# Kernel optimization log

Hardware: AMD Instinct MI355X
Metric: run time of the kernel (lower is better)

Reference implementation:

```python
import jax, jax.numpy as jnp
import numpy as np

N = 262144
D = 6
M = 6
EPS = 1e-05
ALPHA = 0.05


def _w(k, out_dim, in_dim):
    # Kaiming-uniform-ish init like torch Linear default
    bound = 1.0 / np.sqrt(in_dim)
    return jax.random.uniform(k, (out_dim, in_dim), jnp.float32, -bound, bound)


def _b(k, out_dim, in_dim):
    bound = 1.0 / np.sqrt(in_dim)
    return jax.random.uniform(k, (out_dim,), jnp.float32, -bound, bound)


def setup_inputs() -> dict:
    key = jax.random.key(0)
    ks = jax.random.split(key, 32)
    inp = {
        "X": jax.random.normal(ks[0], (N, D), jnp.float32),
        "U": jax.random.normal(ks[1], (N, M), jnp.float32),
        "xref": jax.random.normal(ks[2], (1, D), jnp.float32),
        # FNN: 6 -> 80 -> 200 -> 6
        "fnn_w1": _w(ks[3], 80, D), "fnn_b1": _b(ks[4], 80, D),
        "fnn_w2": _w(ks[5], 200, 80), "fnn_b2": _b(ks[6], 200, 80),
        "fnn_w3": _w(ks[7], D, 200), "fnn_b3": _b(ks[8], D, 200),
        # GNN: 6 -> 36
        "gnn_w": _w(ks[9], D * M, D), "gnn_b": _b(ks[10], D * M, D),
        # ICNN: 6 -> 60 -> 60 -> 30 -> 1 with input skips
        "icnn_w1": _w(ks[11], 60, D), "icnn_b1": _b(ks[12], 60, D),
        "icnn_w2": _w(ks[13], 60, 60), "icnn_b2": _b(ks[14], 60, 60),
        "icnn_w3": _w(ks[15], 30, 60), "icnn_b3": _b(ks[16], 30, 60),
        "icnn_w4": _w(ks[17], 1, 30), "icnn_b4": _b(ks[18], 1, 30),
        "icnn_im2": _w(ks[19], 60, D),
        "icnn_im3": _w(ks[20], 30, D),
        "icnn_im4": _w(ks[21], 1, D),
    }
    return inp


def reference(X, U, xref,
              fnn_w1, fnn_b1, fnn_w2, fnn_b2, fnn_w3, fnn_b3,
              gnn_w, gnn_b,
              icnn_w1, icnn_b1, icnn_w2, icnn_b2, icnn_w3, icnn_b3,
              icnn_w4, icnn_b4, icnn_im2, icnn_im3, icnn_im4):
    def lin(x, W, b=None):
        y = x @ W.T
        return y if b is None else y + b

    def icnn(x):  # (n, D) -> (n, 1)
        h = jax.nn.softplus(lin(x, icnn_w1, icnn_b1))
        h = jax.nn.softplus(lin(h, icnn_w2, icnn_b2) + lin(x, icnn_im2))
        h = jax.nn.softplus(lin(h, icnn_w3, icnn_b3) + lin(x, icnn_im3))
        return lin(h, icnn_w4, icnn_b4) + lin(x, icnn_im4)

    def V_fn(Xb):  # (n, D) -> (n,)
        h = icnn(Xb)[:, 0] - icnn(xref)[0, 0]
        # sigma(h) = (h>=1)(h-0.5) + (0<h<1)(0.5 h^2)
        sigma = jnp.where(h >= 1.0, h - 0.5,
                          jnp.where(h > 0.0, 0.5 * h * h, 0.0))
        dx = Xb - xref
        return sigma + EPS * jnp.sum(dx * dx, axis=1)

    # FNN (tanh hiddens)
    h = jnp.tanh(lin(X, fnn_w1, fnn_b1))
    h = jnp.tanh(lin(h, fnn_w2, fnn_b2))
    f_X = lin(h, fnn_w3, fnn_b3)  # (N, D)

    # GNN
    g_X = lin(X, gnn_w, gnn_b).reshape(X.shape[0], D, M)  # (N, D, M)

    # Lyapunov value and its gradient (per-sample, via grad of summed V)
    V = V_fn(X)  # (N,)
    dV = jax.grad(lambda Z: jnp.sum(V_fn(Z)))(X)  # (N, D)

    # Stability correction
    sc = jnp.sum(dV * f_X, axis=1) + ALPHA * V
    sc = sc - jnp.sum(jnp.abs(jnp.einsum('nd,ndm->nm', dV, g_X)), axis=1)
    dV_norm = dV / jnp.sum(dV * dV, axis=1, keepdims=True)
    f_cor = -dV_norm * jax.nn.relu(sc)[:, None]

    dX_opt = f_X + f_cor + jnp.einsum('ndm,nm->nd', g_X, U)
    return dX_opt
```

## Files before the change

### kernel.cpp

```cpp
#include <hip/hip_runtime.h>

#define EPS 1e-05f
#define ALPHA 0.05f

typedef _Float16 h2v __attribute__((ext_vector_type(2)));
typedef _Float16 f16x8 __attribute__((ext_vector_type(8)));
typedef float f32x16 __attribute__((ext_vector_type(16)));

__device__ __forceinline__ float rcp_f(float x){ return __builtin_amdgcn_rcpf(x); }
__device__ __forceinline__ float dot2(h2v a, h2v b, float c){
  return __builtin_amdgcn_fdot2(a, b, c, false);
}

#define LOG2E 1.4426950408889634f
#define LN2   0.6931471805599453f

__device__ __forceinline__ float fast_tanh(float x){
  float ax = fabsf(x);
  float e  = exp2f(ax * (-2.0f * LOG2E));
  float t  = (1.0f - e) * rcp_f(1.0f + e);
  return copysignf(t, x);
}
__device__ __forceinline__ float fast_sp(float x){
  float ax = fabsf(x);
  float e  = exp2f(ax * -LOG2E);
  return fmaxf(x, 0.0f) + log2f(1.0f + e) * LN2;
}
__device__ __forceinline__ float fast_sig(float x){
  float ax = fabsf(x);
  float e  = exp2f(ax * -LOG2E);
  float r  = rcp_f(1.0f + e);
  return x >= 0.0f ? r : e * r;
}
__device__ __forceinline__ float sig_from_sp(float sp){
  return 1.0f - exp2f(sp * -LOG2E);
}
__device__ __forceinline__ h2v mkh2(float a, float b){
  h2v r; r.x = (_Float16)a; r.y = (_Float16)b; return r;
}
__device__ __forceinline__ uint packh(float a, float b){
  ushort lo = __builtin_bit_cast(ushort, (_Float16)a);
  ushort hi = __builtin_bit_cast(ushort, (_Float16)b);
  return (uint)lo | ((uint)hi << 16);
}
__device__ __forceinline__ float f16lo(uint u){
  return (float)__builtin_bit_cast(_Float16, (ushort)(u & 0xffffu));
}
__device__ __forceinline__ float f16hi(uint u){
  return (float)__builtin_bit_cast(_Float16, (ushort)(u >> 16));
}

__global__ __launch_bounds__(512, 2) void holo_main(
    const float* __restrict__ X, const float* __restrict__ U,
    const float* __restrict__ xref,
    const float* __restrict__ fw1, const float* __restrict__ fb1,
    const float* __restrict__ fw2, const float* __restrict__ fb2,
    const float* __restrict__ fw3, const float* __restrict__ fb3,
    const float* __restrict__ gw,  const float* __restrict__ gb,
    const float* __restrict__ iw1, const float* __restrict__ ib1,
    const float* __restrict__ iw2, const float* __restrict__ ib2,
    const float* __restrict__ iw3, const float* __restrict__ ib3,
    const float* __restrict__ iw4, const float* __restrict__ ib4,
    const float* __restrict__ im2, const float* __restrict__ im3,
    const float* __restrict__ im4,
    float* __restrict__ out, int N)
{
  __shared__ ushort sW2r[224*84];
  __shared__ uint4  sW3r[224];
  __shared__ h2v sPW1[240];
  __shared__ h2v sPG[108];
  __shared__ h2v sPI1[180];
  __shared__ h2v sPI1C[180];
  __shared__ h2v sPI3[900];
  __shared__ h2v sPI3C[900];
  __shared__ h2v sPM2[180];
  __shared__ h2v sPM2C[180];
  __shared__ h2v sPM3[90];
  __shared__ h2v sPM3C[90];
  __shared__ h2v sPM4[4];
  __shared__ h2v sPI2T[1800];
  __shared__ h2v sPI2C[1800];
  __shared__ float sFB1[80], sFB3[6], sGB[36];
  __shared__ float sIB1[60], sIB2[60], sIB3[30], sIW4[30], sIM4[6], sXREF[6];
  __shared__ float sS1[60], sS2[60], sS3[30];
  __shared__ float sYREF, sIB4;

  const int t = threadIdx.x;
  const int T = 512;
  const int lane = t & 63;

  for (int idx=t; idx<224*42; idx+=T){
    int row = idx/42, c = idx%42, k = 2*c;
    uint v = 0;
    if (row < 200 && k < 80) v = packh(fw2[row*80+k], fw2[row*80+k+1]);
    ((uint*)sW2r)[idx] = v;
  }
  for (int n=t; n<224; n+=T){
    uint4 v = {0u,0u,0u,0u};
    if (n < 200){
      v.x = packh(fw3[0*200+n], fw3[1*200+n]);
      v.y = packh(fw3[2*200+n], fw3[3*200+n]);
      v.z = packh(fw3[4*200+n], fw3[5*200+n]);
      v.w = __builtin_bit_cast(uint, fb2[n]);
    }
    sW3r[n] = v;
  }
  for (int i=t;i<240;i+=T){ int o=i/3,p=i%3; sPW1[i]=mkh2(fw1[o*6+2*p],fw1[o*6+2*p+1]); }
  for (int i=t;i<108;i+=T){ int o=i/3,p=i%3; sPG[i]=mkh2(gw[o*6+2*p],gw[o*6+2*p+1]); }
  for (int i=t;i<180;i+=T){ int o=i/3,p=i%3; sPI1[i]=mkh2(iw1[o*6+2*p],iw1[o*6+2*p+1]); }
  for (int i=t;i<180;i+=T){ int q=i/6,d=i%6; sPI1C[i]=mkh2(iw1[(2*q)*6+d],iw1[(2*q+1)*6+d]); }
  for (int i=t;i<900;i+=T){ int r=i/30,q=i%30; sPI3[i]=mkh2(iw3[r*60+2*q],iw3[r*60+2*q+1]); }
  for (int i=t;i<900;i+=T){ int j=i/15,q=i%15; sPI3C[i]=mkh2(iw3[(2*q)*60+j],iw3[(2*q+1)*60+j]); }
  for (int i=t;i<180;i+=T){ int j=i/3,p=i%3; sPM2[i]=mkh2(im2[j*6+2*p],im2[j*6+2*p+1]); }
  for (int i=t;i<180;i+=T){ int q=i/6,d=i%6; sPM2C[i]=mkh2(im2[(2*q)*6+d],im2[(2*q+1)*6+d]); }
  for (int i=t;i<90;i+=T){ int r=i/3,p=i%3; sPM3[i]=mkh2(im3[r*6+2*p],im3[r*6+2*p+1]); }
  for (int i=t;i<90;i+=T){ int q=i/6,d=i%6; sPM3C[i]=mkh2(im3[(2*q)*6+d],im3[(2*q+1)*6+d]); }
  for (int i=t;i<3;i+=T) sPM4[i]=mkh2(im4[2*i],im4[2*i+1]);
  for (int i=t;i<1800;i+=T){ int p=i/60,j=i%60; sPI2T[i]=mkh2(iw2[j*60+2*p],iw2[j*60+2*p+1]); }
  for (int i=t;i<1800;i+=T){ int k1=i/30,q=i%30; sPI2C[i]=mkh2(iw2[(2*q)*60+k1],iw2[(2*q+1)*60+k1]); }
  for (int k=t;k<80;k+=T) sFB1[k]=fb1[k];
  for (int k=t;k<6;k+=T){ sFB3[k]=fb3[k]; sIM4[k]=im4[k]; sXREF[k]=xref[k]; }
  for (int k=t;k<36;k+=T) sGB[k]=gb[k];
  for (int k=t;k<60;k+=T){ sIB1[k]=ib1[k]; sIB2[k]=ib2[k]; }
  for (int k=t;k<30;k+=T){ sIB3[k]=ib3[k]; sIW4[k]=iw4[k]; }
  if (t==0) sIB4=ib4[0];
  __syncthreads();

  {
    h2v xrp[3];
    #pragma unroll
    for (int p = 0; p < 3; p++) xrp[p] = mkh2(sXREF[2*p], sXREF[2*p+1]);
    if (t < 60){
      float z = sIB1[t];
      #pragma unroll
      for (int p = 0; p < 3; p++) z = dot2(sPI1[t*3+p], xrp[p], z);
      sS1[t] = fast_sp(z);
    }
    __syncthreads();
    if (t < 60){
      float z = sIB2[t];
      #pragma unroll
      for (int p = 0; p < 3; p++) z = dot2(sPM2[t*3+p], xrp[p], z);
      for (int p = 0; p < 30; p++)
        z = dot2(sPI2T[p*60+t], mkh2(sS1[2*p], sS1[2*p+1]), z);
      sS2[t] = fast_sp(z);
    }
    __syncthreads();
    if (t < 30){
      float z = sIB3[t];
      #pragma unroll
      for (int p = 0; p < 3; p++) z = dot2(sPM3[t*3+p], xrp[p], z);
      for (int q = 0; q < 30; q++)
        z = dot2(sPI3[t*30+q], mkh2(sS2[2*q], sS2[2*q+1]), z);
      sS3[t] = fast_sp(z);
    }
    __syncthreads();
    if (t == 0){
      float y = sIB4;
      #pragma unroll
      for (int p = 0; p < 3; p++) y = dot2(sPM4[p], xrp[p], y);
      for (int j = 0; j < 30; j++) y = fmaf(sIW4[j], sS3[j], y);
      sYREF = y;
    }
    __syncthreads();
  }

  const int i = blockIdx.x * blockDim.x + t;
  const bool valid = (i < N);

  float x[6]; h2v xp[3];
  #pragma unroll
  for (int k = 0; k < 6; k++) x[k] = valid ? X[(long)i*6 + k] : 0.0f;
  #pragma unroll
  for (int p = 0; p < 3; p++) xp[p] = mkh2(x[2*p], x[2*p+1]);

  uint h1u[40];
  #pragma unroll
  for (int o = 0; o < 80; o += 2){
    float z0 = sFB1[o], z1 = sFB1[o+1];
    #pragma unroll
    for (int p = 0; p < 3; p++){
      z0 = dot2(sPW1[o*3 + p],     xp[p], z0);
      z1 = dot2(sPW1[(o+1)*3 + p], xp[p], z1);
    }
    h1u[o/2] = packh(fast_tanh(z0), fast_tanh(z1));
  }

  const int hh = lane >> 5;
  const int l31 = lane & 31;

  uint bf0[5][4], bf1[5][4];
  {
    int a0 = 4 * l31;
    int a1 = 4 * (32 + l31);
    #pragma unroll
    for (int kt = 0; kt < 5; kt++){
      #pragma unroll
      for (int q = 0; q < 4; q++){
        int lo0 = __builtin_amdgcn_ds_bpermute(a0, (int)h1u[kt*8 + q]);
        int hi0 = __builtin_amdgcn_ds_bpermute(a0, (int)h1u[kt*8 + 4 + q]);
        bf0[kt][q] = hh ? (uint)hi0 : (uint)lo0;
        int lo1 = __builtin_amdgcn_ds_bpermute(a1, (int)h1u[kt*8 + q]);
        int hi1 = __builtin_amdgcn_ds_bpermute(a1, (int)h1u[kt*8 + 4 + q]);
        bf1[kt][q] = hh ? (uint)hi1 : (uint)lo1;
      }
    }
  }

  float fp0[6] = {0.f,0.f,0.f,0.f,0.f,0.f};
  float fp1[6] = {0.f,0.f,0.f,0.f,0.f,0.f};
  for (int mt = 0; mt < 7; mt++){
    const int row = mt*32 + l31;
    f16x8 af[5];
    #pragma unroll
    for (int kt = 0; kt < 5; kt++){
      const ushort* wp = &sW2r[row*84 + kt*16 + 8*hh];
      uint2 w0 = *(const uint2*)wp;
      uint2 w1 = *(const uint2*)(wp + 4);
      uint4 au; au.x = w0.x; au.y = w0.y; au.z = w1.x; au.w = w1.y;
      af[kt] = __builtin_bit_cast(f16x8, au);
    }
    f32x16 acc0 = {0,0,0,0,0,0,0,0,0,0,0,0,0,0,0,0};
    f32x16 acc1 = {0,0,0,0,0,0,0,0,0,0,0,0,0,0,0,0};
    #pragma unroll
    for (int kt = 0; kt < 5; kt++){
      uint4 b0u; b0u.x=bf0[kt][0]; b0u.y=bf0[kt][1]; b0u.z=bf0[kt][2]; b0u.w=bf0[kt][3];
      uint4 b1u; b1u.x=bf1[kt][0]; b1u.y=bf1[kt][1]; b1u.z=bf1[kt][2]; b1u.w=bf1[kt][3];
      acc0 = __builtin_amdgcn_mfma_f32_32x32x16_f16(af[kt], __builtin_bit_cast(f16x8, b0u), acc0, 0, 0, 0);
      acc1 = __builtin_amdgcn_mfma_f32_32x32x16_f16(af[kt], __builtin_bit_cast(f16x8, b1u), acc1, 0, 0, 0);
    }
    #pragma unroll
    for (int reg = 0; reg < 16; reg++){
      int n = mt*32 + (reg & 3) + 8*(reg >> 2) + 4*hh;
      uint4 w = sW3r[n];
      float bias = __builtin_bit_cast(float, w.w);
      float t0 = fast_tanh(acc0[reg] + bias);
      float t1 = fast_tanh(acc1[reg] + bias);
      float w0 = f16lo(w.x), w1 = f16hi(w.x);
      float w2 = f16lo(w.y), w3 = f16hi(w.y);
      float w4 = f16lo(w.z), w5 = f16hi(w.z);
      fp0[0] = fmaf(w0, t0, fp0[0]); fp1[0] = fmaf(w0, t1, fp1[0]);
      fp0[1] = fmaf(w1, t0, fp0[1]); fp1[1] = fmaf(w1, t1, fp1[1]);
      fp0[2] = fmaf(w2, t0, fp0[2]); fp1[2] = fmaf(w2, t1, fp1[2]);
      fp0[3] = fmaf(w3, t0, fp0[3]); fp1[3] = fmaf(w3, t1, fp1[3]);
      fp0[4] = fmaf(w4, t0, fp0[4]); fp1[4] = fmaf(w4, t1, fp1[4]);
      fp0[5] = fmaf(w5, t0, fp0[5]); fp1[5] = fmaf(w5, t1, fp1[5]);
    }
  }
  float f[6];
  #pragma unroll
  for (int d = 0; d < 6; d++){
    float s0 = fp0[d] + __shfl_xor(fp0[d], 32, 64);
    float s1 = fp1[d] + __shfl_xor(fp1[d], 32, 64);
    f[d] = sFB3[d] + (hh ? s1 : s0);
  }

  float c2[60];
  #pragma unroll
  for (int j = 0; j < 60; j++){
    float z = sIB2[j];
    #pragma unroll
    for (int p = 0; p < 3; p++) z = dot2(sPM2[j*3 + p], xp[p], z);
    c2[j] = z;
  }
  for (int p = 0; p < 30; p++){
    float za = sIB1[2*p], zb = sIB1[2*p+1];
    #pragma unroll
    for (int q = 0; q < 3; q++){
      za = dot2(sPI1[(2*p)*3 + q],   xp[q], za);
      zb = dot2(sPI1[(2*p+1)*3 + q], xp[q], zb);
    }
    h2v s = mkh2(fast_sp(za), fast_sp(zb));
    #pragma unroll
    for (int j = 0; j < 60; j++) c2[j] = dot2(sPI2T[p*60 + j], s, c2[j]);
  }
  h2v c2p[30];
  #pragma unroll
  for (int j = 0; j < 60; j += 2)
    c2p[j/2] = mkh2(fast_sp(c2[j]), fast_sp(c2[j+1]));

  float y = sIB4;
  #pragma unroll
  for (int p = 0; p < 3; p++) y = dot2(sPM4[p], xp[p], y);
  float ac[6];
  #pragma unroll
  for (int d = 0; d < 6; d++) ac[d] = sIM4[d];
  float g3[30];
  #pragma unroll
  for (int i3 = 0; i3 < 30; i3++){
    float z = sIB3[i3];
    #pragma unroll
    for (int p = 0; p < 3; p++) z = dot2(sPM3[i3*3 + p], xp[p], z);
    #pragma unroll
    for (int q = 0; q < 30; q++) z = dot2(sPI3[i3*30 + q], c2p[q], z);
    float sp3 = fast_sp(z);
    float w4  = sIW4[i3];
    y = fmaf(w4, sp3, y);
    g3[i3] = w4 * sig_from_sp(sp3);
  }
  h2v g3p[15];
  #pragma unroll
  for (int q = 0; q < 15; q++) g3p[q] = mkh2(g3[2*q], g3[2*q+1]);
  #pragma unroll
  for (int q = 0; q < 15; q++){
    #pragma unroll
    for (int d = 0; d < 6; d++) ac[d] = dot2(sPM3C[q*6 + d], g3p[q], ac[d]);
  }

  h2v g2p[30];
  #pragma unroll
  for (int j = 0; j < 60; j += 2){
    float ta = 0.0f, tb = 0.0f;
    #pragma unroll
    for (int q = 0; q < 15; q++){
      ta = dot2(sPI3C[j*15 + q],     g3p[q], ta);
      tb = dot2(sPI3C[(j+1)*15 + q], g3p[q], tb);
    }
    h2v sp = c2p[j/2];
    ta *= sig_from_sp((float)sp.x);
    tb *= sig_from_sp((float)sp.y);
    h2v tp = mkh2(ta, tb);
    g2p[j/2] = tp;
    #pragma unroll
    for (int d = 0; d < 6; d++) ac[d] = dot2(sPM2C[(j/2)*6 + d], tp, ac[d]);
  }

  for (int p = 0; p < 30; p++){
    float za = sIB1[2*p], zb = sIB1[2*p+1];
    #pragma unroll
    for (int q = 0; q < 3; q++){
      za = dot2(sPI1[(2*p)*3 + q],   xp[q], za);
      zb = dot2(sPI1[(2*p+1)*3 + q], xp[q], zb);
    }
    float ta = 0.0f, tb = 0.0f;
    #pragma unroll
    for (int q = 0; q < 30; q++){
      ta = dot2(sPI2C[(2*p)*30 + q],   g2p[q], ta);
      tb = dot2(sPI2C[(2*p+1)*30 + q], g2p[q], tb);
    }
    ta *= fast_sig(za); tb *= fast_sig(zb);
    h2v tp = mkh2(ta, tb);
    #pragma unroll
    for (int d = 0; d < 6; d++) ac[d] = dot2(sPI1C[p*6 + d], tp, ac[d]);
  }

  float hdiff = y - sYREF;
  float sigma = (hdiff >= 1.0f) ? (hdiff - 0.5f) : ((hdiff > 0.0f) ? 0.5f*hdiff*hdiff : 0.0f);
  float sigp  = (hdiff >= 1.0f) ? 1.0f          : ((hdiff > 0.0f) ? hdiff             : 0.0f);
  float dx2 = 0.0f;
  float dV[6];
  #pragma unroll
  for (int d = 0; d < 6; d++){
    float dx = x[d] - sXREF[d];
    dx2 = fmaf(dx, dx, dx2);
    dV[d] = fmaf(sigp, ac[d], 2.0f*EPS*dx);
  }
  float V = sigma + EPS*dx2;

  float sc = ALPHA * V;
  #pragma unroll
  for (int d = 0; d < 6; d++) sc = fmaf(dV[d], f[d], sc);

  float u[6];
  #pragma unroll
  for (int m = 0; m < 6; m++) u[m] = valid ? U[(long)i*6 + m] : 0.0f;
  float am[6] = {0.f,0.f,0.f,0.f,0.f,0.f};
  float gU[6];
  #pragma unroll
  for (int d = 0; d < 6; d++){
    float acc = 0.0f;
    #pragma unroll
    for (int m = 0; m < 6; m++){
      int o = d*6 + m;
      float g = sGB[o];
      #pragma unroll
      for (int p = 0; p < 3; p++) g = dot2(sPG[o*3 + p], xp[p], g);
      am[m] = fmaf(dV[d], g, am[m]);
      acc   = fmaf(g, u[m], acc);
    }
    gU[d] = acc;
  }
  #pragma unroll
  for (int m = 0; m < 6; m++) sc -= fabsf(am[m]);

  float n2 = 0.0f;
  #pragma unroll
  for (int d = 0; d < 6; d++) n2 = fmaf(dV[d], dV[d], n2);
  float r = fmaxf(sc, 0.0f) * rcp_f(n2);

  if (valid){
    #pragma unroll
    for (int d = 0; d < 6; d++)
      out[(long)i*6 + d] = f[d] - dV[d]*r + gU[d];
  }
}

extern "C" void kernel_launch(void* const* d_in, const int* in_sizes, int n_in,
                              void* d_out, int out_size, void* d_ws, size_t ws_size,
                              hipStream_t stream)
{
  const float* X    = (const float*)d_in[0];
  const float* U    = (const float*)d_in[1];
  const float* xref = (const float*)d_in[2];
  const float* fw1  = (const float*)d_in[3];
  const float* fb1  = (const float*)d_in[4];
  const float* fw2  = (const float*)d_in[5];
  const float* fb2  = (const float*)d_in[6];
  const float* fw3  = (const float*)d_in[7];
  const float* fb3  = (const float*)d_in[8];
  const float* gw   = (const float*)d_in[9];
  const float* gb   = (const float*)d_in[10];
  const float* iw1  = (const float*)d_in[11];
  const float* ib1  = (const float*)d_in[12];
  const float* iw2  = (const float*)d_in[13];
  const float* ib2  = (const float*)d_in[14];
  const float* iw3  = (const float*)d_in[15];
  const float* ib3  = (const float*)d_in[16];
  const float* iw4  = (const float*)d_in[17];
  const float* ib4  = (const float*)d_in[18];
  const float* im2  = (const float*)d_in[19];
  const float* im3  = (const float*)d_in[20];
  const float* im4  = (const float*)d_in[21];

  float* out = (float*)d_out;
  int N = in_sizes[0] / 6;

  int threads = 512;
  int blocks  = (N + threads - 1) / threads;
  holo_main<<<blocks, threads, 0, stream>>>(X, U, xref,
      fw1, fb1, fw2, fb2, fw3, fb3, gw, gb,
      iw1, ib1, iw2, ib2, iw3, ib3, iw4, ib4, im2, im3, im4,
      out, N);
}
```

Baseline: 182.8 us.

## Repack shared-memory weights into 16-byte padded records for vectorized LDS reads

Repacks all small weight tables in LDS as padded uint4 records that carry their biases, so each row or bias group comes in with one 128-bit LDS load instead of many scalar 32-bit loads. The FNN output projection now packs tanh pairs into half2 and accumulates with fdot2, replacing scalar f16-to-f32 conversions and FMAs. This cuts LDS instruction count in the per-thread ICNN forward/backward chain. The cost is some zero padding in LDS and a longer one-time packing prologue per block.

```diff
diff --git a/kernel.cpp b/kernel.cpp
--- a/kernel.cpp
+++ b/kernel.cpp
@@ -11,6 +11,8 @@
 __device__ __forceinline__ float dot2(h2v a, h2v b, float c){
   return __builtin_amdgcn_fdot2(a, b, c, false);
 }
+__device__ __forceinline__ h2v uh(uint u){ return __builtin_bit_cast(h2v, u); }
+__device__ __forceinline__ float uf(uint u){ return __builtin_bit_cast(float, u); }
 
 #define LOG2E 1.4426950408889634f
 #define LN2   0.6931471805599453f
@@ -42,12 +44,6 @@
   ushort lo = __builtin_bit_cast(ushort, (_Float16)a);
   ushort hi = __builtin_bit_cast(ushort, (_Float16)b);
   return (uint)lo | ((uint)hi << 16);
-}
-__device__ __forceinline__ float f16lo(uint u){
-  return (float)__builtin_bit_cast(_Float16, (ushort)(u & 0xffffu));
-}
-__device__ __forceinline__ float f16hi(uint u){
-  return (float)__builtin_bit_cast(_Float16, (ushort)(u >> 16));
 }
 
 __global__ __launch_bounds__(512, 2) void holo_main(
@@ -65,23 +61,22 @@
     const float* __restrict__ im4,
     float* __restrict__ out, int N)
 {
-  __shared__ ushort sW2r[224*84];
-  __shared__ uint4  sW3r[224];
-  __shared__ h2v sPW1[240];
-  __shared__ h2v sPG[108];
-  __shared__ h2v sPI1[180];
-  __shared__ h2v sPI1C[180];
-  __shared__ h2v sPI3[900];
-  __shared__ h2v sPI3C[900];
-  __shared__ h2v sPM2[180];
-  __shared__ h2v sPM2C[180];
-  __shared__ h2v sPM3[90];
-  __shared__ h2v sPM3C[90];
-  __shared__ h2v sPM4[4];
-  __shared__ h2v sPI2T[1800];
-  __shared__ h2v sPI2C[1800];
-  __shared__ float sFB1[80], sFB3[6], sGB[36];
-  __shared__ float sIB1[60], sIB2[60], sIB3[30], sIW4[30], sIM4[6], sXREF[6];
+  __shared__ alignas(16) ushort sW2r[224*84];
+  __shared__ uint4 sW3E[224];
+  __shared__ uint4 sPW1B[80];
+  __shared__ uint4 sPGB[36];
+  __shared__ uint4 sPI1B[60];
+  __shared__ uint4 sPI1C[60];
+  __shared__ uint4 sPI3[240];
+  __shared__ uint4 sPI3C[240];
+  __shared__ uint4 sPM2B[60];
+  __shared__ uint4 sPM2C[60];
+  __shared__ uint4 sPM3B[60];
+  __shared__ uint4 sPM3C[30];
+  __shared__ uint  sPM4u[4];
+  __shared__ alignas(16) uint sPI2Tu[1800];
+  __shared__ uint4 sPI2C[480];
+  __shared__ float sFB3[6], sXREF[6], sIM4[6];
   __shared__ float sS1[60], sS2[60], sS3[30];
   __shared__ float sYREF, sIB4;
 
@@ -95,34 +90,75 @@
     if (row < 200 && k < 80) v = packh(fw2[row*80+k], fw2[row*80+k+1]);
     ((uint*)sW2r)[idx] = v;
   }
-  for (int n=t; n<224; n+=T){
-    uint4 v = {0u,0u,0u,0u};
+  for (int idx=t; idx<896; idx+=T){
+    int P = idx/8, c = idx%8, n = 2*P;
+    uint v = 0;
     if (n < 200){
-      v.x = packh(fw3[0*200+n], fw3[1*200+n]);
-      v.y = packh(fw3[2*200+n], fw3[3*200+n]);
-      v.z = packh(fw3[4*200+n], fw3[5*200+n]);
-      v.w = __builtin_bit_cast(uint, fb2[n]);
-    }
-    sW3r[n] = v;
-  }
-  for (int i=t;i<240;i+=T){ int o=i/3,p=i%3; sPW1[i]=mkh2(fw1[o*6+2*p],fw1[o*6+2*p+1]); }
-  for (int i=t;i<108;i+=T){ int o=i/3,p=i%3; sPG[i]=mkh2(gw[o*6+2*p],gw[o*6+2*p+1]); }
-  for (int i=t;i<180;i+=T){ int o=i/3,p=i%3; sPI1[i]=mkh2(iw1[o*6+2*p],iw1[o*6+2*p+1]); }
-  for (int i=t;i<180;i+=T){ int q=i/6,d=i%6; sPI1C[i]=mkh2(iw1[(2*q)*6+d],iw1[(2*q+1)*6+d]); }
-  for (int i=t;i<900;i+=T){ int r=i/30,q=i%30; sPI3[i]=mkh2(iw3[r*60+2*q],iw3[r*60+2*q+1]); }
-  for (int i=t;i<900;i+=T){ int j=i/15,q=i%15; sPI3C[i]=mkh2(iw3[(2*q)*60+j],iw3[(2*q+1)*60+j]); }
-  for (int i=t;i<180;i+=T){ int j=i/3,p=i%3; sPM2[i]=mkh2(im2[j*6+2*p],im2[j*6+2*p+1]); }
-  for (int i=t;i<180;i+=T){ int q=i/6,d=i%6; sPM2C[i]=mkh2(im2[(2*q)*6+d],im2[(2*q+1)*6+d]); }
-  for (int i=t;i<90;i+=T){ int r=i/3,p=i%3; sPM3[i]=mkh2(im3[r*6+2*p],im3[r*6+2*p+1]); }
-  for (int i=t;i<90;i+=T){ int q=i/6,d=i%6; sPM3C[i]=mkh2(im3[(2*q)*6+d],im3[(2*q+1)*6+d]); }
-  for (int i=t;i<3;i+=T) sPM4[i]=mkh2(im4[2*i],im4[2*i+1]);
-  for (int i=t;i<1800;i+=T){ int p=i/60,j=i%60; sPI2T[i]=mkh2(iw2[j*60+2*p],iw2[j*60+2*p+1]); }
-  for (int i=t;i<1800;i+=T){ int k1=i/30,q=i%30; sPI2C[i]=mkh2(iw2[(2*q)*60+k1],iw2[(2*q+1)*60+k1]); }
-  for (int k=t;k<80;k+=T) sFB1[k]=fb1[k];
+      if (c < 6)       v = packh(fw3[c*200+n], fw3[c*200+n+1]);
+      else if (c == 6) v = __builtin_bit_cast(uint, fb2[n]);
+      else             v = __builtin_bit_cast(uint, fb2[n+1]);
+    }
+    ((uint*)sW3E)[idx] = v;
+  }
+  for (int idx=t; idx<320; idx+=T){
+    int o = idx/4, c = idx%4;
+    ((uint*)sPW1B)[idx] = (c<3) ? packh(fw1[o*6+2*c], fw1[o*6+2*c+1])
+                                : __builtin_bit_cast(uint, fb1[o]);
+  }
+  for (int idx=t; idx<144; idx+=T){
+    int o = idx/4, c = idx%4;
+    ((uint*)sPGB)[idx] = (c<3) ? packh(gw[o*6+2*c], gw[o*6+2*c+1])
+                               : __builtin_bit_cast(uint, gb[o]);
+  }
+  for (int idx=t; idx<240; idx+=T){
+    int p = idx/8, c = idx%8, sub = c/4, cc = c%4, nr = 2*p+sub;
+    ((uint*)sPI1B)[idx] = (cc<3) ? packh(iw1[nr*6+2*cc], iw1[nr*6+2*cc+1])
+                                 : __builtin_bit_cast(uint, ib1[nr]);
+  }
+  for (int idx=t; idx<240; idx+=T){
+    int q = idx/8, c = idx%8;
+    ((uint*)sPI1C)[idx] = (c<6) ? packh(iw1[(2*q)*6+c], iw1[(2*q+1)*6+c]) : 0u;
+  }
+  for (int idx=t; idx<960; idx+=T){
+    int r = idx/32, q = idx%32;
+    ((uint*)sPI3)[idx] = (q<30) ? packh(iw3[r*60+2*q], iw3[r*60+2*q+1]) : 0u;
+  }
+  for (int idx=t; idx<960; idx+=T){
+    int j = idx/16, q = idx%16;
+    ((uint*)sPI3C)[idx] = (q<15) ? packh(iw3[(2*q)*60+j], iw3[(2*q+1)*60+j]) : 0u;
+  }
+  for (int idx=t; idx<240; idx+=T){
+    int j = idx/4, c = idx%4;
+    ((uint*)sPM2B)[idx] = (c<3) ? packh(im2[j*6+2*c], im2[j*6+2*c+1])
+                                : __builtin_bit_cast(uint, ib2[j]);
+  }
+  for (int idx=t; idx<240; idx+=T){
+    int q = idx/8, c = idx%8;
+    ((uint*)sPM2C)[idx] = (c<6) ? packh(im2[(2*q)*6+c], im2[(2*q+1)*6+c]) : 0u;
+  }
+  for (int idx=t; idx<240; idx+=T){
+    int r = idx/8, c = idx%8;
+    uint v = 0;
+    if (c < 3)       v = packh(im3[r*6+2*c], im3[r*6+2*c+1]);
+    else if (c == 3) v = __builtin_bit_cast(uint, ib3[r]);
+    else if (c == 4) v = __builtin_bit_cast(uint, iw4[r]);
+    ((uint*)sPM3B)[idx] = v;
+  }
+  for (int idx=t; idx<120; idx+=T){
+    int q = idx/8, c = idx%8;
+    ((uint*)sPM3C)[idx] = (c<6) ? packh(im3[(2*q)*6+c], im3[(2*q+1)*6+c]) : 0u;
+  }
+  for (int idx=t; idx<4; idx+=T)
+    sPM4u[idx] = (idx<3) ? packh(im4[2*idx], im4[2*idx+1]) : 0u;
+  for (int idx=t; idx<1800; idx+=T){
+    int p = idx/60, j = idx%60;
+    sPI2Tu[idx] = packh(iw2[j*60+2*p], iw2[j*60+2*p+1]);
+  }
+  for (int idx=t; idx<1920; idx+=T){
+    int k1 = idx/32, q = idx%32;
+    ((uint*)sPI2C)[idx] = (q<30) ? packh(iw2[(2*q)*60+k1], iw2[(2*q+1)*60+k1]) : 0u;
+  }
   for (int k=t;k<6;k+=T){ sFB3[k]=fb3[k]; sIM4[k]=im4[k]; sXREF[k]=xref[k]; }
-  for (int k=t;k<36;k+=T) sGB[k]=gb[k];
-  for (int k=t;k<60;k+=T){ sIB1[k]=ib1[k]; sIB2[k]=ib2[k]; }
-  for (int k=t;k<30;k+=T){ sIB3[k]=ib3[k]; sIW4[k]=iw4[k]; }
   if (t==0) sIB4=ib4[0];
   __syncthreads();
 
@@ -131,35 +167,39 @@
     #pragma unroll
     for (int p = 0; p < 3; p++) xrp[p] = mkh2(sXREF[2*p], sXREF[2*p+1]);
     if (t < 60){
-      float z = sIB1[t];
+      const uint* w = (const uint*)sPI1B + (t/2)*8 + (t&1)*4;
+      float z = uf(w[3]);
       #pragma unroll
-      for (int p = 0; p < 3; p++) z = dot2(sPI1[t*3+p], xrp[p], z);
+      for (int c = 0; c < 3; c++) z = dot2(uh(w[c]), xrp[c], z);
       sS1[t] = fast_sp(z);
     }
     __syncthreads();
     if (t < 60){
-      float z = sIB2[t];
+      const uint* m = (const uint*)sPM2B + t*4;
+      float z = uf(m[3]);
       #pragma unroll
-      for (int p = 0; p < 3; p++) z = dot2(sPM2[t*3+p], xrp[p], z);
+      for (int c = 0; c < 3; c++) z = dot2(uh(m[c]), xrp[c], z);
       for (int p = 0; p < 30; p++)
-        z = dot2(sPI2T[p*60+t], mkh2(sS1[2*p], sS1[2*p+1]), z);
+        z = dot2(uh(sPI2Tu[p*60+t]), mkh2(sS1[2*p], sS1[2*p+1]), z);
       sS2[t] = fast_sp(z);
     }
     __syncthreads();
     if (t < 30){
-      float z = sIB3[t];
+      const uint* m = (const uint*)sPM3B + t*8;
+      float z = uf(m[3]);
       #pragma unroll
-      for (int p = 0; p < 3; p++) z = dot2(sPM3[t*3+p], xrp[p], z);
+      for (int c = 0; c < 3; c++) z = dot2(uh(m[c]), xrp[c], z);
+      const uint* prow = (const uint*)sPI3 + t*32;
       for (int q = 0; q < 30; q++)
-        z = dot2(sPI3[t*30+q], mkh2(sS2[2*q], sS2[2*q+1]), z);
+        z = dot2(uh(prow[q]), mkh2(sS2[2*q], sS2[2*q+1]), z);
       sS3[t] = fast_sp(z);
     }
     __syncthreads();
     if (t == 0){
       float y = sIB4;
       #pragma unroll
-      for (int p = 0; p < 3; p++) y = dot2(sPM4[p], xrp[p], y);
-      for (int j = 0; j < 30; j++) y = fmaf(sIW4[j], sS3[j], y);
+      for (int p = 0; p < 3; p++) y = dot2(uh(sPM4u[p]), xrp[p], y);
+      for (int j = 0; j < 30; j++) y = fmaf(uf(((const uint*)sPM3B)[j*8+4]), sS3[j], y);
       sYREF = y;
     }
     __syncthreads();
@@ -177,12 +217,10 @@
   uint h1u[40];
   #pragma unroll
   for (int o = 0; o < 80; o += 2){
-    float z0 = sFB1[o], z1 = sFB1[o+1];
-    #pragma unroll
-    for (int p = 0; p < 3; p++){
-      z0 = dot2(sPW1[o*3 + p],     xp[p], z0);
-      z1 = dot2(sPW1[(o+1)*3 + p], xp[p], z1);
-    }
+    uint4 wa = sPW1B[o], wb = sPW1B[o+1];
+    float z0 = uf(wa.w), z1 = uf(wb.w);
+    z0 = dot2(uh(wa.x), xp[0], z0); z0 = dot2(uh(wa.y), xp[1], z0); z0 = dot2(uh(wa.z), xp[2], z0);
+    z1 = dot2(uh(wb.x), xp[0], z1); z1 = dot2(uh(wb.y), xp[1], z1); z1 = dot2(uh(wb.z), xp[2], z1);
     h1u[o/2] = packh(fast_tanh(z0), fast_tanh(z1));
   }
 
@@ -230,21 +268,22 @@
       acc1 = __builtin_amdgcn_mfma_f32_32x32x16_f16(af[kt], __builtin_bit_cast(f16x8, b1u), acc1, 0, 0, 0);
     }
     #pragma unroll
-    for (int reg = 0; reg < 16; reg++){
-      int n = mt*32 + (reg & 3) + 8*(reg >> 2) + 4*hh;
-      uint4 w = sW3r[n];
-      float bias = __builtin_bit_cast(float, w.w);
-      float t0 = fast_tanh(acc0[reg] + bias);
-      float t1 = fast_tanh(acc1[reg] + bias);
-      float w0 = f16lo(w.x), w1 = f16hi(w.x);
-      float w2 = f16lo(w.y), w3 = f16hi(w.y);
-      float w4 = f16lo(w.z), w5 = f16hi(w.z);
-      fp0[0] = fmaf(w0, t0, fp0[0]); fp1[0] = fmaf(w0, t1, fp1[0]);
-      fp0[1] = fmaf(w1, t0, fp0[1]); fp1[1] = fmaf(w1, t1, fp1[1]);
-      fp0[2] = fmaf(w2, t0, fp0[2]); fp1[2] = fmaf(w2, t1, fp1[2]);
-      fp0[3] = fmaf(w3, t0, fp0[3]); fp1[3] = fmaf(w3, t1, fp1[3]);
-      fp0[4] = fmaf(w4, t0, fp0[4]); fp1[4] = fmaf(w4, t1, fp1[4]);
-      fp0[5] = fmaf(w5, t0, fp0[5]); fp1[5] = fmaf(w5, t1, fp1[5]);
+    for (int c = 0; c < 4; c++){
+      #pragma unroll
+      for (int b0h = 0; b0h < 2; b0h++){
+        const int r0 = 4*c + 2*b0h;
+        const int P  = mt*16 + 4*c + 2*hh + b0h;
+        uint4 wa = sW3E[P*2], wb = sW3E[P*2+1];
+        float bA = uf(wb.z), bB = uf(wb.w);
+        h2v tp0 = mkh2(fast_tanh(acc0[r0] + bA), fast_tanh(acc0[r0+1] + bB));
+        h2v tp1 = mkh2(fast_tanh(acc1[r0] + bA), fast_tanh(acc1[r0+1] + bB));
+        fp0[0] = dot2(uh(wa.x), tp0, fp0[0]); fp1[0] = dot2(uh(wa.x), tp1, fp1[0]);
+        fp0[1] = dot2(uh(wa.y), tp0, fp0[1]); fp1[1] = dot2(uh(wa.y), tp1, fp1[1]);
+        fp0[2] = dot2(uh(wa.z), tp0, fp0[2]); fp1[2] = dot2(uh(wa.z), tp1, fp1[2]);
+        fp0[3] = dot2(uh(wa.w), tp0, fp0[3]); fp1[3] = dot2(uh(wa.w), tp1, fp1[3]);
+        fp0[4] = dot2(uh(wb.x), tp0, fp0[4]); fp1[4] = dot2(uh(wb.x), tp1, fp1[4]);
+        fp0[5] = dot2(uh(wb.y), tp0, fp0[5]); fp1[5] = dot2(uh(wb.y), tp1, fp1[5]);
+      }
     }
   }
   float f[6];
@@ -258,90 +297,136 @@
   float c2[60];
   #pragma unroll
   for (int j = 0; j < 60; j++){
-    float z = sIB2[j];
-    #pragma unroll
-    for (int p = 0; p < 3; p++) z = dot2(sPM2[j*3 + p], xp[p], z);
+    uint4 m = sPM2B[j];
+    float z = uf(m.w);
+    z = dot2(uh(m.x), xp[0], z); z = dot2(uh(m.y), xp[1], z); z = dot2(uh(m.z), xp[2], z);
     c2[j] = z;
   }
   for (int p = 0; p < 30; p++){
-    float za = sIB1[2*p], zb = sIB1[2*p+1];
-    #pragma unroll
-    for (int q = 0; q < 3; q++){
-      za = dot2(sPI1[(2*p)*3 + q],   xp[q], za);
-      zb = dot2(sPI1[(2*p+1)*3 + q], xp[q], zb);
-    }
+    uint4 wA = sPI1B[2*p], wB = sPI1B[2*p+1];
+    float za = uf(wA.w), zb = uf(wB.w);
+    za = dot2(uh(wA.x), xp[0], za); za = dot2(uh(wA.y), xp[1], za); za = dot2(uh(wA.z), xp[2], za);
+    zb = dot2(uh(wB.x), xp[0], zb); zb = dot2(uh(wB.y), xp[1], zb); zb = dot2(uh(wB.z), xp[2], zb);
     h2v s = mkh2(fast_sp(za), fast_sp(zb));
-    #pragma unroll
-    for (int j = 0; j < 60; j++) c2[j] = dot2(sPI2T[p*60 + j], s, c2[j]);
-  }
-  h2v c2p[30];
+    const uint* rowp = sPI2Tu + p*60;
+    #pragma unroll
+    for (int jj = 0; jj < 15; jj++){
+      uint4 v = *(const uint4*)(rowp + jj*4);
+      c2[4*jj+0] = dot2(uh(v.x), s, c2[4*jj+0]);
+      c2[4*jj+1] = dot2(uh(v.y), s, c2[4*jj+1]);
+      c2[4*jj+2] = dot2(uh(v.z), s, c2[4*jj+2]);
+      c2[4*jj+3] = dot2(uh(v.w), s, c2[4*jj+3]);
+    }
+  }
+  h2v c2p[32];
   #pragma unroll
   for (int j = 0; j < 60; j += 2)
     c2p[j/2] = mkh2(fast_sp(c2[j]), fast_sp(c2[j+1]));
+  c2p[30] = mkh2(0.f, 0.f); c2p[31] = mkh2(0.f, 0.f);
 
   float y = sIB4;
   #pragma unroll
-  for (int p = 0; p < 3; p++) y = dot2(sPM4[p], xp[p], y);
+  for (int p = 0; p < 3; p++) y = dot2(uh(sPM4u[p]), xp[p], y);
   float ac[6];
   #pragma unroll
   for (int d = 0; d < 6; d++) ac[d] = sIM4[d];
   float g3[30];
   #pragma unroll
   for (int i3 = 0; i3 < 30; i3++){
-    float z = sIB3[i3];
-    #pragma unroll
-    for (int p = 0; p < 3; p++) z = dot2(sPM3[i3*3 + p], xp[p], z);
-    #pragma unroll
-    for (int q = 0; q < 30; q++) z = dot2(sPI3[i3*30 + q], c2p[q], z);
+    uint4 m0 = sPM3B[2*i3], m1 = sPM3B[2*i3+1];
+    float z = uf(m0.w);
+    z = dot2(uh(m0.x), xp[0], z); z = dot2(uh(m0.y), xp[1], z); z = dot2(uh(m0.z), xp[2], z);
+    const uint4* prow = sPI3 + i3*8;
+    #pragma unroll
+    for (int q4 = 0; q4 < 8; q4++){
+      uint4 v = prow[q4];
+      z = dot2(uh(v.x), c2p[4*q4+0], z);
+      z = dot2(uh(v.y), c2p[4*q4+1], z);
+      z = dot2(uh(v.z), c2p[4*q4+2], z);
+      z = dot2(uh(v.w), c2p[4*q4+3], z);
+    }
     float sp3 = fast_sp(z);
-    float w4  = sIW4[i3];
+    float w4  = uf(m1.x);
     y = fmaf(w4, sp3, y);
     g3[i3] = w4 * sig_from_sp(sp3);
   }
-  h2v g3p[15];
+  h2v g3p[16];
   #pragma unroll
   for (int q = 0; q < 15; q++) g3p[q] = mkh2(g3[2*q], g3[2*q+1]);
+  g3p[15] = mkh2(0.f, 0.f);
   #pragma unroll
   for (int q = 0; q < 15; q++){
-    #pragma unroll
-    for (int d = 0; d < 6; d++) ac[d] = dot2(sPM3C[q*6 + d], g3p[q], ac[d]);
-  }
-
-  h2v g2p[30];
-  #pragma unroll
-  for (int j = 0; j < 60; j += 2){
+    uint4 a = sPM3C[2*q], b = sPM3C[2*q+1];
+    ac[0] = dot2(uh(a.x), g3p[q], ac[0]);
+    ac[1] = dot2(uh(a.y), g3p[q], ac[1]);
+    ac[2] = dot2(uh(a.z), g3p[q], ac[2]);
+    ac[3] = dot2(uh(a.w), g3p[q], ac[3]);
+    ac[4] = dot2(uh(b.x), g3p[q], ac[4]);
+    ac[5] = dot2(uh(b.y), g3p[q], ac[5]);
+  }
+
+  h2v g2p[32];
+  #pragma unroll
+  for (int jp = 0; jp < 30; jp++){
+    const uint4* r0p = sPI3C + (2*jp)*4;
+    const uint4* r1p = sPI3C + (2*jp+1)*4;
     float ta = 0.0f, tb = 0.0f;
     #pragma unroll
-    for (int q = 0; q < 15; q++){
-      ta = dot2(sPI3C[j*15 + q],     g3p[q], ta);
-      tb = dot2(sPI3C[(j+1)*15 + q], g3p[q], tb);
-    }
-    h2v sp = c2p[j/2];
+    for (int q4 = 0; q4 < 4; q4++){
+      uint4 v0 = r0p[q4], v1 = r1p[q4];
+      ta = dot2(uh(v0.x), g3p[4*q4+0], ta);
+      ta = dot2(uh(v0.y), g3p[4*q4+1], ta);
+      ta = dot2(uh(v0.z), g3p[4*q4+2], ta);
+      ta = dot2(uh(v0.w), g3p[4*q4+3], ta);
+      tb = dot2(uh(v1.x), g3p[4*q4+0], tb);
+      tb = dot2(uh(v1.y), g3p[4*q4+1], tb);
+      tb = dot2(uh(v1.z), g3p[4*q4+2], tb);
+      tb = dot2(uh(v1.w), g3p[4*q4+3], tb);
+    }
+    h2v sp = c2p[jp];
     ta *= sig_from_sp((float)sp.x);
     tb *= sig_from_sp((float)sp.y);
     h2v tp = mkh2(ta, tb);
-    g2p[j/2] = tp;
-    #pragma unroll
-    for (int d = 0; d < 6; d++) ac[d] = dot2(sPM2C[(j/2)*6 + d], tp, ac[d]);
-  }
+    g2p[jp] = tp;
+    uint4 a = sPM2C[2*jp], b = sPM2C[2*jp+1];
+    ac[0] = dot2(uh(a.x), tp, ac[0]);
+    ac[1] = dot2(uh(a.y), tp, ac[1]);
+    ac[2] = dot2(uh(a.z), tp, ac[2]);
+    ac[3] = dot2(uh(a.w), tp, ac[3]);
+    ac[4] = dot2(uh(b.x), tp, ac[4]);
+    ac[5] = dot2(uh(b.y), tp, ac[5]);
+  }
+  g2p[30] = mkh2(0.f, 0.f); g2p[31] = mkh2(0.f, 0.f);
 
   for (int p = 0; p < 30; p++){
-    float za = sIB1[2*p], zb = sIB1[2*p+1];
-    #pragma unroll
-    for (int q = 0; q < 3; q++){
-      za = dot2(sPI1[(2*p)*3 + q],   xp[q], za);
-      zb = dot2(sPI1[(2*p+1)*3 + q], xp[q], zb);
-    }
+    uint4 wA = sPI1B[2*p], wB = sPI1B[2*p+1];
+    float za = uf(wA.w), zb = uf(wB.w);
+    za = dot2(uh(wA.x), xp[0], za); za = dot2(uh(wA.y), xp[1], za); za = dot2(uh(wA.z), xp[2], za);
+    zb = dot2(uh(wB.x), xp[0], zb); zb = dot2(uh(wB.y), xp[1], zb); zb = dot2(uh(wB.z), xp[2], zb);
+    const uint4* c0 = sPI2C + (2*p)*8;
+    const uint4* c1 = sPI2C + (2*p+1)*8;
     float ta = 0.0f, tb = 0.0f;
     #pragma unroll
-    for (int q = 0; q < 30; q++){
-      ta = dot2(sPI2C[(2*p)*30 + q],   g2p[q], ta);
-      tb = dot2(sPI2C[(2*p+1)*30 + q], g2p[q], tb);
+    for (int q4 = 0; q4 < 8; q4++){
+      uint4 v0 = c0[q4], v1 = c1[q4];
+      ta = dot2(uh(v0.x), g2p[4*q4+0], ta);
+      ta = dot2(uh(v0.y), g2p[4*q4+1], ta);
+      ta = dot2(uh(v0.z), g2p[4*q4+2], ta);
+      ta = dot2(uh(v0.w), g2p[4*q4+3], ta);
+      tb = dot2(uh(v1.x), g2p[4*q4+0], tb);
+      tb = dot2(uh(v1.y), g2p[4*q4+1], tb);
+      tb = dot2(uh(v1.z), g2p[4*q4+2], tb);
+      tb = dot2(uh(v1.w), g2p[4*q4+3], tb);
     }
     ta *= fast_sig(za); tb *= fast_sig(zb);
     h2v tp = mkh2(ta, tb);
-    #pragma unroll
-    for (int d = 0; d < 6; d++) ac[d] = dot2(sPI1C[p*6 + d], tp, ac[d]);
+    uint4 a = sPI1C[2*p], b = sPI1C[2*p+1];
+    ac[0] = dot2(uh(a.x), tp, ac[0]);
+    ac[1] = dot2(uh(a.y), tp, ac[1]);
+    ac[2] = dot2(uh(a.z), tp, ac[2]);
+    ac[3] = dot2(uh(a.w), tp, ac[3]);
+    ac[4] = dot2(uh(b.x), tp, ac[4]);
+    ac[5] = dot2(uh(b.y), tp, ac[5]);
   }
 
   float hdiff = y - sYREF;
@@ -372,9 +457,9 @@
     #pragma unroll
     for (int m = 0; m < 6; m++){
       int o = d*6 + m;
-      float g = sGB[o];
-      #pragma unroll
-      for (int p = 0; p < 3; p++) g = dot2(sPG[o*3 + p], xp[p], g);
+      uint4 g4 = sPGB[o];
+      float g = uf(g4.w);
+      g = dot2(uh(g4.x), xp[0], g); g = dot2(uh(g4.y), xp[1], g); g = dot2(uh(g4.z), xp[2], g);
       am[m] = fmaf(dV[d], g, am[m]);
       acc   = fmaf(g, u[m], acc);
     }
```

After: 198.3 us. 1.08x slower.
